# Optimization experiments

Hardware: AMD Instinct MI355X
Metric: run time of the kernel (lower is better)

## Reference

```python
import jax, jax.numpy as jnp
import numpy as np
import math

T = 4096
HID = 2048
H = 16
D = 128
RD = 64            # rotary_dim = head_dim * partial_rotary_factor (0.5)
THETA = 10000.0
EPS = 1e-6
GROUPS = 8
LAYER_IDX = 2
N_LAYERS = 32


def build_slope_tensor(num_heads):
    def get_slopes_power_of_2(n):
        start = 2 ** (-(2 ** (-(math.log2(n) - 3))))
        ratio = start
        return [start * ratio ** i for i in range(n)]
    if math.log2(num_heads).is_integer():
        return get_slopes_power_of_2(num_heads)
    closest = 2 ** math.floor(math.log2(num_heads))
    return (get_slopes_power_of_2(closest)
            + build_slope_tensor(2 * closest)[0::2][: num_heads - closest])


def compute_slope():
    base = np.array(build_slope_tensor(H), dtype=np.float32)
    return jnp.asarray(-base * (1 - (LAYER_IDX - 1) / (N_LAYERS - 1) + 1e-5), dtype=jnp.float32)


def setup_inputs() -> dict:
    key = jax.random.key(0)
    ks = jax.random.split(key, 8)
    s = 0.02
    return {
        "positions": jnp.arange(T, dtype=jnp.int32),
        "hidden_states": jax.random.normal(ks[0], (T, HID), dtype=jnp.float32),
        "recurrent_state": jnp.zeros((1, H, D, D), dtype=jnp.float32),
        "w_qkv": jax.random.normal(ks[1], (HID, 3 * H * D), dtype=jnp.float32) * s,
        "w_g": jax.random.normal(ks[2], (HID, H * D), dtype=jnp.float32) * s,
        "w_dense": jax.random.normal(ks[3], (H * D, HID), dtype=jnp.float32) * s,
        "q_norm_w": jnp.ones((D,), dtype=jnp.float32),
        "k_norm_w": jnp.ones((D,), dtype=jnp.float32),
        "g_norm_w": jnp.ones((H * D,), dtype=jnp.float32),
    }


def _rms(x, w):
    var = jnp.mean(jnp.square(x), axis=-1, keepdims=True)
    return x * jax.lax.rsqrt(var + EPS) * w


def _rope(x, positions):
    # partial neox-style rotary on first RD dims of each head
    inv_freq = 1.0 / (THETA ** (jnp.arange(0, RD, 2, dtype=jnp.float32) / RD))
    freqs = positions.astype(jnp.float32)[:, None] * inv_freq   # [T, RD/2]
    cos = jnp.cos(freqs)[:, None, :]                            # [T, 1, RD/2]
    sin = jnp.sin(freqs)[:, None, :]
    x1 = x[..., : RD // 2]
    x2 = x[..., RD // 2 : RD]
    x_pass = x[..., RD:]
    return jnp.concatenate([x1 * cos - x2 * sin, x2 * cos + x1 * sin, x_pass], axis=-1)


def reference(positions, hidden_states, recurrent_state,
              w_qkv, w_g, w_dense, q_norm_w, k_norm_w, g_norm_w):
    t = hidden_states.shape[0]
    qkv = (hidden_states @ w_qkv).reshape(t, 3, H, D)
    q, k, v = qkv[:, 0], qkv[:, 1], qkv[:, 2]
    q = _rms(q, q_norm_w)
    k = _rms(k, k_norm_w)
    q = _rope(q, positions)
    k = _rope(k, positions)

    slope = compute_slope()                    # [H], negative
    decay = jnp.exp(slope)                     # per-head per-step decay
    scale = D ** -0.5
    q = (q * scale).astype(jnp.float32)
    k = k.astype(jnp.float32)
    v = v.astype(jnp.float32)

    def step(S, qkv_t):
        q_t, k_t, v_t = qkv_t                  # each [H, D]
        S = S * decay[:, None, None] + k_t[:, :, None] * v_t[:, None, :]
        o_t = jnp.einsum('hk,hkv->hv', q_t, S)
        return S, o_t

    S0 = recurrent_state[0].astype(jnp.float32)   # [H, K, V]
    S_final, o = jax.lax.scan(step, S0, (q, k, v))
    attn = o.reshape(t, H * D)

    gate = jax.nn.sigmoid(hidden_states @ w_g)
    # GroupRMSNorm: normalize per group of size (H*D)/GROUPS, scale by full weight
    g = attn.reshape(t, GROUPS, (H * D) // GROUPS)
    var = jnp.mean(jnp.square(g), axis=-1, keepdims=True)
    g = (g * jax.lax.rsqrt(var + EPS)).reshape(t, H * D) * g_norm_w

    out = (g * gate) @ w_dense
    return out, S_final[None]
```

## Files before the change

### kernel.cpp

```cpp
#include <hip/hip_runtime.h>
#include <hip/hip_bf16.h>

using bf16x8 = __attribute__((ext_vector_type(8))) __bf16;
using f32x4  = __attribute__((ext_vector_type(4))) float;

constexpr int T_SEQ = 4096;
constexpr int HID_C = 2048;
constexpr int NH    = 16;
constexpr int QKV_N = 6144;

__device__ __forceinline__ float head_slope(int h) {
    return -exp2f(-0.5f * (float)(h + 1)) * 0.967751935483871f;
}

__device__ __forceinline__ ushort f2bfu(float f) {
    __hip_bfloat16 h = __float2bfloat16(f);
    return *(ushort*)&h;
}
__device__ __forceinline__ float bfu2f(ushort u) {
    union { unsigned int i; float f; } x; x.i = ((unsigned int)u) << 16; return x.f;
}

__device__ __forceinline__ void async16(const ushort* g, ushort* l) {
    __builtin_amdgcn_global_load_lds((const __attribute__((address_space(1))) void*)g,
                                     (__attribute__((address_space(3))) void*)l, 16, 0, 0);
}

template<int N> __device__ __forceinline__ void waitcnt_vm() {
    if constexpr (N == 0)      asm volatile("s_waitcnt vmcnt(0)" ::: "memory");
    else if constexpr (N == 2) asm volatile("s_waitcnt vmcnt(2)" ::: "memory");
    else if constexpr (N == 4) asm volatile("s_waitcnt vmcnt(4)" ::: "memory");
    else if constexpr (N == 6) asm volatile("s_waitcnt vmcnt(6)" ::: "memory");
}

__device__ __forceinline__ void cvt_body(const float* __restrict__ src, ushort* __restrict__ dst,
                                         int bid, int tid) {
    int i = (bid * 256 + tid) * 8;
    float4 a = *(const float4*)(src + i);
    float4 b = *(const float4*)(src + i + 4);
    ushort4 ua = {f2bfu(a.x), f2bfu(a.y), f2bfu(a.z), f2bfu(a.w)};
    ushort4 ub = {f2bfu(b.x), f2bfu(b.y), f2bfu(b.z), f2bfu(b.w)};
    *(ushort4*)(dst + i) = ua;
    *(ushort4*)(dst + i + 4) = ub;
}

__device__ __forceinline__ void transpose_body(const float* __restrict__ src,
                                               ushort* __restrict__ dst,
                                               int R, int C, int bx, int by, int t,
                                               ushort (*tile)[68]) {
    int tr = by * 64, tc = bx * 64;
    int r0 = t >> 4;
    int c4 = (t & 15) << 2;
#pragma unroll
    for (int p = 0; p < 4; ++p) {
        int row = r0 + p * 16;
        float4 v = *(const float4*)&src[(size_t)(tr + row) * C + tc + c4];
        tile[row][c4 + 0] = f2bfu(v.x);
        tile[row][c4 + 1] = f2bfu(v.y);
        tile[row][c4 + 2] = f2bfu(v.z);
        tile[row][c4 + 3] = f2bfu(v.w);
    }
    __syncthreads();
#pragma unroll
    for (int p = 0; p < 4; ++p) {
        int orow = r0 + p * 16;
        ushort4 u;
        u.x = tile[c4 + 0][orow];
        u.y = tile[c4 + 1][orow];
        u.z = tile[c4 + 2][orow];
        u.w = tile[c4 + 3][orow];
        *(ushort4*)&dst[(size_t)(tc + orow) * R + tr + c4] = u;
    }
}

__global__ __launch_bounds__(256) void prep_all(const float* __restrict__ hidden,
                                                ushort* __restrict__ hid_b,
                                                const float* __restrict__ w_qkv,
                                                ushort* __restrict__ wqkv_t,
                                                const float* __restrict__ w_g,
                                                ushort* __restrict__ wg_t,
                                                const float* __restrict__ w_dense,
                                                ushort* __restrict__ wd_t,
                                                const int* __restrict__ positions,
                                                float2* __restrict__ ropet) {
    __shared__ ushort tile[64][68];
    int b = blockIdx.x, t = threadIdx.x;
    if (b < 4096) {
        cvt_body(hidden, hid_b, b, t);
    } else if (b < 7168) {
        int bb = b - 4096;
        transpose_body(w_qkv, wqkv_t, HID_C, QKV_N, bb % 96, bb / 96, t, tile);
    } else if (b < 8192) {
        int bb = b - 7168;
        transpose_body(w_g, wg_t, HID_C, HID_C, bb % 32, bb / 32, t, tile);
    } else if (b < 9216) {
        int bb = b - 8192;
        transpose_body(w_dense, wd_t, HID_C, HID_C, bb % 32, bb / 32, t, tile);
    } else {
        int i = (b - 9216) * 256 + t;
        int tt = i >> 5, fi = i & 31;
        float inv = expf((float)fi * -0.2878231366f);
        float freq = (float)positions[tt] * inv;
        float sn, cs;
        sincosf(freq, &sn, &cs);
        ropet[i] = make_float2(cs, sn);
    }
}

template<int MI, int BN>
__device__ __forceinline__ void gemm8_core(const ushort* __restrict__ Ag,
                                           const ushort* __restrict__ Bg,
                                           int K, int bm, int bn,
                                           ushort* sh, f32x4 (&acc)[MI][4]) {
    constexpr int WM = 16 / MI;
    constexpr int WN = 8 / WM;
    constexpr int SB = BN / 128;
    constexpr int AH = (MI >= 8) ? 2 : 1;
    constexpr int MH = MI / AH;

    const int tid  = threadIdx.x;
    const int lane = tid & 63;
    const int wave = tid >> 6;
    const int lane15 = lane & 15, quad = lane >> 4;
    const int wm = wave / WN, wn = wave % WN;
    const int swz = lane15 & 7;

    ushort* const ldsA0 = sh;
    ushort* const ldsA1 = sh + 16384;
    ushort* const ldsB0 = sh + 32768;
    ushort* const ldsB1 = sh + 32768 + BN * 64;

    const int srow = lane >> 3;
    const int scol = ((lane & 7) ^ srow) << 3;
    const ushort* gA = Ag + (size_t)(bm + srow) * K + scol;
    const ushort* gB = Bg + (size_t)(bn + srow) * K + scol;
    const int ro  = wave * 16;
    const int roB = wave * 8 * SB;
    const int NT = K >> 6;

#define STAGE_A(L, k0) do { \
    _Pragma("unroll") for (int h = 0; h < 2; ++h) \
    _Pragma("unroll") for (int q = 0; q < 2; ++q) \
        async16(gA + (size_t)((h) * 128 + ro + q * 8) * K + (k0), (L) + ((h) * 128 + ro + q * 8) * 64); } while (0)
#define STAGE_B(L, k0) do { \
    _Pragma("unroll") for (int h = 0; h < 2; ++h) \
    _Pragma("unroll") for (int q = 0; q < SB; ++q) \
        async16(gB + (size_t)((h) * (BN / 2) + roB + q * 8) * K + (k0), (L) + ((h) * (BN / 2) + roB + q * 8) * 64); } while (0)

    STAGE_A(ldsA0, 0);
    STAGE_B(ldsB0, 0);
    waitcnt_vm<0>();
    asm volatile("s_barrier" ::: "memory");

    for (int t = 0; t < NT; ++t) {
        const ushort* LA = (t & 1) ? ldsA1 : ldsA0;
        const ushort* LB = (t & 1) ? ldsB1 : ldsB0;
        ushort* LAn = (t & 1) ? ldsA0 : ldsA1;
        ushort* LBn = (t & 1) ? ldsB0 : ldsB1;
        bf16x8 bfr[4][2];
#pragma unroll
        for (int j = 0; j < 4; ++j)
#pragma unroll
            for (int ks = 0; ks < 2; ++ks)
                bfr[j][ks] = *(const bf16x8*)&LB[(wn * 64 + j * 16 + lane15) * 64 + (((ks * 4 + quad) ^ swz) << 3)];
        bf16x8 af0[MH][2];
#pragma unroll
        for (int i = 0; i < MH; ++i)
#pragma unroll
            for (int ks = 0; ks < 2; ++ks)
                af0[i][ks] = *(const bf16x8*)&LA[(wm * (MI * 16) + i * 16 + lane15) * 64 + (((ks * 4 + quad) ^ swz) << 3)];
        if (t + 1 < NT) {
            STAGE_A(LAn, (t + 1) << 6);
            STAGE_B(LBn, (t + 1) << 6);
        }
        __builtin_amdgcn_s_setprio(1);
#pragma unroll
        for (int i = 0; i < MH; ++i)
#pragma unroll
            for (int j = 0; j < 4; ++j)
#pragma unroll
                for (int ks = 0; ks < 2; ++ks)
                    acc[i][j] = __builtin_amdgcn_mfma_f32_16x16x32_bf16(af0[i][ks], bfr[j][ks], acc[i][j], 0, 0, 0);
        __builtin_amdgcn_s_setprio(0);
        if constexpr (AH == 2) {
            bf16x8 af1[MH][2];
#pragma unroll
            for (int i = 0; i < MH; ++i)
#pragma unroll
                for (int ks = 0; ks < 2; ++ks)
                    af1[i][ks] = *(const bf16x8*)&LA[(wm * (MI * 16) + (MH + i) * 16 + lane15) * 64 + (((ks * 4 + quad) ^ swz) << 3)];
            __builtin_amdgcn_s_setprio(1);
#pragma unroll
            for (int i = 0; i < MH; ++i)
#pragma unroll
                for (int j = 0; j < 4; ++j)
#pragma unroll
                    for (int ks = 0; ks < 2; ++ks)
                        acc[MH + i][j] = __builtin_amdgcn_mfma_f32_16x16x32_bf16(af1[i][ks], bfr[j][ks], acc[MH + i][j], 0, 0, 0);
            __builtin_amdgcn_s_setprio(0);
        }
        waitcnt_vm<0>();
        asm volatile("s_barrier" ::: "memory");
    }
#undef STAGE_A
#undef STAGE_B
}

__device__ __forceinline__ void gemm4_core(const ushort* __restrict__ Ag,
                                           const ushort* __restrict__ Bg,
                                           int K, int bm, int bn,
                                           ushort* sh, f32x4 (&acc)[4][4]) {
    const int tid  = threadIdx.x;
    const int lane = tid & 63;
    const int wave = tid >> 6;
    const int lane15 = lane & 15, quad = lane >> 4;
    const int wm = wave >> 1, wn = wave & 1;
    const int swz = lane15 & 7;

    ushort* const ldsA0 = sh;
    ushort* const ldsA1 = sh + 8192;
    ushort* const ldsB0 = sh + 16384;
    ushort* const ldsB1 = sh + 24576;

    const int srow = lane >> 3;
    const int scol = ((lane & 7) ^ srow) << 3;
    const ushort* gA = Ag + (size_t)(bm + srow) * K + scol;
    const ushort* gB = Bg + (size_t)(bn + srow) * K + scol;
    const int ro = wave * 32;
    const int NT = K >> 6;

#define STG(L, g, k0) do { \
    _Pragma("unroll") for (int q = 0; q < 4; ++q) \
        async16((g) + (size_t)(ro + q * 8) * K + (k0), (L) + (ro + q * 8) * 64); } while (0)

    STG(ldsA0, gA, 0);
    STG(ldsB0, gB, 0);
    waitcnt_vm<0>();
    asm volatile("s_barrier" ::: "memory");

    for (int t = 0; t < NT; ++t) {
        const ushort* LA = (t & 1) ? ldsA1 : ldsA0;
        const ushort* LB = (t & 1) ? ldsB1 : ldsB0;
        ushort* LAn = (t & 1) ? ldsA0 : ldsA1;
        ushort* LBn = (t & 1) ? ldsB0 : ldsB1;
        bf16x8 bfr[4][2];
#pragma unroll
        for (int j = 0; j < 4; ++j)
#pragma unroll
            for (int ks = 0; ks < 2; ++ks)
                bfr[j][ks] = *(const bf16x8*)&LB[(wn * 64 + j * 16 + lane15) * 64 + (((ks * 4 + quad) ^ swz) << 3)];
        bf16x8 af[4][2];
#pragma unroll
        for (int i = 0; i < 4; ++i)
#pragma unroll
            for (int ks = 0; ks < 2; ++ks)
                af[i][ks] = *(const bf16x8*)&LA[(wm * 64 + i * 16 + lane15) * 64 + (((ks * 4 + quad) ^ swz) << 3)];
        if (t + 1 < NT) {
            STG(LAn, gA, (t + 1) << 6);
            STG(LBn, gB, (t + 1) << 6);
        }
        __builtin_amdgcn_s_setprio(1);
#pragma unroll
        for (int i = 0; i < 4; ++i)
#pragma unroll
            for (int j = 0; j < 4; ++j)
#pragma unroll
                for (int ks = 0; ks < 2; ++ks)
                    acc[i][j] = __builtin_amdgcn_mfma_f32_16x16x32_bf16(af[i][ks], bfr[j][ks], acc[i][j], 0, 0, 0);
        __builtin_amdgcn_s_setprio(0);
        waitcnt_vm<0>();
        asm volatile("s_barrier" ::: "memory");
    }
#undef STG
}

__global__ __launch_bounds__(512, 2) void gemm_fused(const ushort* __restrict__ A,
                                                     const ushort* __restrict__ Bcat,
                                                     ushort* __restrict__ qkv,
                                                     ushort* __restrict__ gate,
                                                     ushort* __restrict__ vT, int K) {
    __shared__ ushort sh[65536];
    int bid = blockIdx.x;
    int x = bid & 7, w = bid >> 3;
    int rm = x >> 2, rn = x & 3;
    int wm_i = w >> 3, wn_i = w & 7;
    int bm = (rm * 8 + wm_i) * 256;
    int bn = (rn * 8 + wn_i) * 256;
    f32x4 acc[8][4] = {};
    gemm8_core<8, 256>(A, Bcat, K, bm, bn, sh, acc);

    int lane = threadIdx.x & 63, wave = threadIdx.x >> 6;
    int lane15 = lane & 15, quad = lane >> 4;
    int wm = wave >> 2, wn = wave & 3;

    if (bn >= 4096 && bn < QKV_N) {
        constexpr int S = 132;
        ushort* L = sh;
        int h0 = (bn - 4096) >> 7;
        int c0 = bm >> 7;
        int hq = wn >> 1;
        int dl = (wn & 1) * 64;
#pragma unroll
        for (int cq = 0; cq < 2; ++cq) {
            if (wm == cq) {
#pragma unroll
                for (int i = 0; i < 8; ++i)
#pragma unroll
                    for (int j = 0; j < 4; ++j) {
                        int d_local = dl + j * 16 + lane15;
#pragma unroll
                        for (int r = 0; r < 4; ++r) {
                            int t_local = i * 16 + quad * 4 + r;
                            L[hq * 128 * S + d_local * S + t_local] = f2bfu(acc[i][j][r]);
                        }
                    }
            }
            __syncthreads();
#pragma unroll
            for (int p = 0; p < 16; ++p) {
                int lin = (p * 512 + threadIdx.x) * 4;
                int hq2 = lin >> 14;
                int wi = lin & 16383;
                int d = wi >> 7, t4 = wi & 127;
                const ushort* lp = &L[hq2 * 128 * S + d * S + t4];
                ushort4 u = { lp[0], lp[1], lp[2], lp[3] };
                *(ushort4*)&vT[((size_t)((h0 + hq2) * 32 + c0 + cq) * 128 + d) * 128 + t4] = u;
            }
            __syncthreads();
        }
        return;
    }

    bool isg = bn >= QKV_N;
    ushort* outp = isg ? gate : qkv;
    int ncol = isg ? HID_C : QKV_N;
    int cb = (isg ? bn - QKV_N : bn) + wn * 64;
    int rb = bm + wm * 128;
#pragma unroll
    for (int i = 0; i < 8; ++i)
#pragma unroll
        for (int j = 0; j < 4; ++j) {
            int col = cb + j * 16 + lane15;
#pragma unroll
            for (int r = 0; r < 4; ++r) {
                float v = acc[i][j][r];
                if (isg) v = 1.0f / (1.0f + __expf(-v));
                outp[(size_t)(rb + i * 16 + quad * 4 + r) * ncol + col] = f2bfu(v);
            }
        }
}

__global__ __launch_bounds__(256, 2) void gemm_dense(const ushort* __restrict__ A,
                                                     const ushort* __restrict__ Bt,
                                                     float* __restrict__ Cout, int N, int K) {
    __shared__ ushort sh[32768];
    int bid = blockIdx.x;
    int x = bid & 7, w = bid >> 3;
    int rm = x >> 1, rn = x & 1;
    int wm_i = w >> 3, wn_i = w & 7;
    int bm = (rm * 8 + wm_i) * 128;
    int bn = (rn * 8 + wn_i) * 128;
    f32x4 acc[4][4] = {};
    gemm4_core(A, Bt, K, bm, bn, sh, acc);

    int lane = threadIdx.x & 63, wave = threadIdx.x >> 6;
    int lane15 = lane & 15, quad = lane >> 4;
    int wm = wave >> 1, wn = wave & 1;
    int cb = bn + wn * 64;
    int rb = bm + wm * 64;
#pragma unroll
    for (int i = 0; i < 4; ++i)
#pragma unroll
        for (int j = 0; j < 4; ++j) {
            int col = cb + j * 16 + lane15;
#pragma unroll
            for (int r = 0; r < 4; ++r)
                Cout[(size_t)(rb + i * 16 + quad * 4 + r) * N + col] = acc[i][j][r];
        }
}

__global__ __launch_bounds__(256) void qk_rope_T(ushort* __restrict__ qkv,
                                                 const float2* __restrict__ tab,
                                                 const float* __restrict__ qw,
                                                 const float* __restrict__ kw,
                                                 ushort* __restrict__ kT) {
    __shared__ ushort tile[64][132];
    int bt = blockIdx.x;
    int kind = blockIdx.y >> 4, h = blockIdx.y & 15;
    int tid = threadIdx.x;
    int row = tid >> 2, c = tid & 3, d0 = c * 32;
    int t = bt * 64 + row;
    ushort* base = qkv + (size_t)t * QKV_N + kind * 2048 + h * 128 + d0;
    bf16x8 pk[4];
#pragma unroll
    for (int p = 0; p < 4; ++p) pk[p] = *(const bf16x8*)(base + p * 8);
    {
        float x[32];
        float ss = 0.f;
#pragma unroll
        for (int p = 0; p < 4; ++p)
#pragma unroll
            for (int i = 0; i < 8; ++i) {
                x[p * 8 + i] = (float)pk[p][i];
                ss += x[p * 8 + i] * x[p * 8 + i];
            }
        ss += __shfl_xor(ss, 1);
        ss += __shfl_xor(ss, 2);
        float rr = rsqrtf(ss * (1.0f / 128.0f) + 1e-6f);
        const float* w = (kind == 0) ? qw : kw;
#pragma unroll
        for (int i = 0; i < 32; ++i) x[i] *= rr * w[d0 + i];
#pragma unroll
        for (int i = 0; i < 32; ++i) {
            float p = __shfl_xor(x[i], 1);
            if (c < 2) {
                float2 rt = tab[t * 32 + i];
                x[i] = (c == 0) ? (x[i] * rt.x - p * rt.y) : (x[i] * rt.x + p * rt.y);
            }
        }
        float sc = (kind == 0) ? 0.08838834764831845f : 1.0f;
#pragma unroll
        for (int p = 0; p < 4; ++p)
#pragma unroll
            for (int i = 0; i < 8; ++i) pk[p][i] = (__bf16)(x[p * 8 + i] * sc);
#pragma unroll
        for (int p = 0; p < 4; ++p) *(bf16x8*)(base + p * 8) = pk[p];
    }
    if (kind == 1) {
#pragma unroll
        for (int p = 0; p < 4; ++p) {
            ushort4* s = (ushort4*)&pk[p];
            *(ushort4*)&tile[row][d0 + p * 8]     = s[0];
            *(ushort4*)&tile[row][d0 + p * 8 + 4] = s[1];
        }
        __syncthreads();
        ushort* outT = kT + ((size_t)(h * 32 + (bt >> 1)) * 128) * 128 + (bt & 1) * 64;
        int d = tid >> 1, half = tid & 1;
#pragma unroll
        for (int tt = 0; tt < 8; ++tt) {
            int tl = half * 32 + tt * 4;
            ushort4 u;
            u.x = tile[tl + 0][d];
            u.y = tile[tl + 1][d];
            u.z = tile[tl + 2][d];
            u.w = tile[tl + 3][d];
            *(ushort4*)&outT[(size_t)d * 128 + tl] = u;
        }
    }
}

__global__ __launch_bounds__(256) void chunk_partial(const ushort* __restrict__ kT,
                                                     const ushort* __restrict__ vT,
                                                     ushort* __restrict__ PT) {
    int c = blockIdx.x, h = blockIdx.y;
    float slope = head_slope(h);
    float lam_inv = __expf(-slope);
    int tid = threadIdx.x, lane = tid & 63, wave = tid >> 6;
    int lane15 = lane & 15, quad = lane >> 4;
    int wv = (wave & 1) * 64, wd = (wave >> 1) * 64;
    const ushort* vbase = vT + ((size_t)(h * 32 + c) * 128) * 128;
    const ushort* kbase = kT + ((size_t)(h * 32 + c) * 128) * 128;
    f32x4 acc[4][4] = {};
#pragma unroll
    for (int j0 = 0; j0 < 128; j0 += 32) {
        float w8[8];
        w8[0] = __expf(slope * (float)(127 - (j0 + quad * 8)));
#pragma unroll
        for (int kk = 1; kk < 8; ++kk) w8[kk] = w8[kk - 1] * lam_inv;
        bf16x8 afr[4], bfr[4];
#pragma unroll
        for (int i = 0; i < 4; ++i) {
            bf16x8 v = *(const bf16x8*)&vbase[(size_t)(wv + i * 16 + lane15) * 128 + j0 + quad * 8];
#pragma unroll
            for (int kk = 0; kk < 8; ++kk) afr[i][kk] = (__bf16)((float)v[kk] * w8[kk]);
        }
#pragma unroll
        for (int j = 0; j < 4; ++j)
            bfr[j] = *(const bf16x8*)&kbase[(size_t)(wd + j * 16 + lane15) * 128 + j0 + quad * 8];
#pragma unroll
        for (int i = 0; i < 4; ++i)
#pragma unroll
            for (int j = 0; j < 4; ++j)
                acc[i][j] = __builtin_amdgcn_mfma_f32_16x16x32_bf16(afr[i], bfr[j], acc[i][j], 0, 0, 0);
    }
    ushort* out = PT + ((size_t)c * 16 + h) * 16384;
#pragma unroll
    for (int i = 0; i < 4; ++i)
#pragma unroll
        for (int j = 0; j < 4; ++j)
#pragma unroll
            for (int r = 0; r < 4; ++r)
                out[(size_t)(wv + i * 16 + quad * 4 + r) * 128 + wd + j * 16 + lane15] = f2bfu(acc[i][j][r]);
}

__global__ __launch_bounds__(128) void scan_states(const ushort* __restrict__ PT,
                                                   const float* __restrict__ S0,
                                                   ushort* __restrict__ Spb,
                                                   float* __restrict__ Sfin) {
    int hv = blockIdx.x;
    int d = threadIdx.x;
    int h = hv >> 7, v = hv & 127;
    float lamC = __expf(head_slope(h) * 128.0f);
    float s = S0[(size_t)h * 16384 + d * 128 + v];
#pragma unroll
    for (int c = 0; c < 32; ++c) {
        size_t idx = ((size_t)c * 2048 + hv) * 128 + d;
        Spb[idx] = f2bfu(s);
        s = s * lamC + bfu2f(PT[idx]);
    }
    Sfin[(size_t)h * 16384 + d * 128 + v] = s;
}

__global__ __launch_bounds__(256) void chunk_out(const ushort* __restrict__ qkv,
                                                 const ushort* __restrict__ vT,
                                                 const ushort* __restrict__ Spb,
                                                 ushort* __restrict__ o) {
    int c = blockIdx.x, h = blockIdx.y;
    float slope = head_slope(h);
    __shared__ ushort Ps[128 * 136];
    int tid = threadIdx.x, lane = tid & 63, wave = tid >> 6;
    int lane15 = lane & 15, quad = lane >> 4;
    int t0 = c * 128;
    int tt0 = wave, tt1 = 7 - wave;
    const ushort* qbase = qkv + (size_t)t0 * QKV_N + h * 128;
    const ushort* kbase = qbase + 2048;

    bf16x8 qf0[4], qf1[4];
#pragma unroll
    for (int ds = 0; ds < 4; ++ds) {
        qf0[ds] = *(const bf16x8*)&qbase[(size_t)(tt0 * 16 + lane15) * QKV_N + ds * 32 + quad * 8];
        qf1[ds] = *(const bf16x8*)&qbase[(size_t)(tt1 * 16 + lane15) * QKV_N + ds * 32 + quad * 8];
    }
    f32x4 s0a[4] = {};
    f32x4 s1a[8] = {};
#pragma unroll
    for (int st = 0; st < 8; ++st) {
        if (st <= tt1) {
            bf16x8 kf[4];
#pragma unroll
            for (int ds = 0; ds < 4; ++ds)
                kf[ds] = *(const bf16x8*)&kbase[(size_t)(st * 16 + lane15) * QKV_N + ds * 32 + quad * 8];
#pragma unroll
            for (int ds = 0; ds < 4; ++ds)
                s1a[st] = __builtin_amdgcn_mfma_f32_16x16x32_bf16(qf1[ds], kf[ds], s1a[st], 0, 0, 0);
            if (st <= tt0) {
#pragma unroll
                for (int ds = 0; ds < 4; ++ds)
                    s0a[st] = __builtin_amdgcn_mfma_f32_16x16x32_bf16(qf0[ds], kf[ds], s0a[st], 0, 0, 0);
            }
        }
    }
    int stmax0 = tt0 + ((tt0 & 1) ? 0 : 1);
    int stmax1 = tt1 + ((tt1 & 1) ? 0 : 1);
#pragma unroll
    for (int st = 0; st < 8; ++st) {
        if (st <= stmax1) {
#pragma unroll
            for (int r = 0; r < 4; ++r) {
                int t = tt1 * 16 + quad * 4 + r;
                int s = st * 16 + lane15;
                float val = 0.f;
                if (st <= tt1) val = (s <= t) ? s1a[st][r] * __expf(slope * (float)(t - s)) : 0.f;
                Ps[t * 136 + s] = f2bfu(val);
            }
        }
    }
#pragma unroll
    for (int st = 0; st < 5; ++st) {
        if (st <= stmax0) {
#pragma unroll
            for (int r = 0; r < 4; ++r) {
                int t = tt0 * 16 + quad * 4 + r;
                int s = st * 16 + lane15;
                float val = 0.f;
                if (st <= tt0) val = (s <= t) ? s0a[st][r] * __expf(slope * (float)(t - s)) : 0.f;
                Ps[t * 136 + s] = f2bfu(val);
            }
        }
    }
    __syncthreads();
    f32x4 oa0[8] = {};
    f32x4 oa1[8] = {};
    float lam0 = __expf(slope * (float)(tt0 * 16 + lane15 + 1));
    float lam1 = __expf(slope * (float)(tt1 * 16 + lane15 + 1));
    bf16x8 qs0[4], qs1[4];
#pragma unroll
    for (int ds = 0; ds < 4; ++ds)
#pragma unroll
        for (int kk = 0; kk < 8; ++kk) {
            qs0[ds][kk] = (__bf16)((float)qf0[ds][kk] * lam0);
            qs1[ds][kk] = (__bf16)((float)qf1[ds][kk] * lam1);
        }
    const ushort* spb = Spb + ((size_t)c * 2048 + h * 128) * 128;
#pragma unroll
    for (int vt = 0; vt < 8; ++vt)
#pragma unroll
        for (int ds = 0; ds < 4; ++ds) {
            bf16x8 bfrag = *(const bf16x8*)&spb[(vt * 16 + lane15) * 128 + ds * 32 + quad * 8];
            oa0[vt] = __builtin_amdgcn_mfma_f32_16x16x32_bf16(qs0[ds], bfrag, oa0[vt], 0, 0, 0);
            oa1[vt] = __builtin_amdgcn_mfma_f32_16x16x32_bf16(qs1[ds], bfrag, oa1[vt], 0, 0, 0);
        }
    const ushort* vbase = vT + ((size_t)(h * 32 + c) * 128) * 128;
    int ns0 = (tt0 + 2) >> 1, ns1 = (tt1 + 2) >> 1;
#pragma unroll
    for (int s32 = 0; s32 < 4; ++s32) {
        if (s32 < ns1) {
            bf16x8 af = *(const bf16x8*)&Ps[(tt1 * 16 + lane15) * 136 + s32 * 32 + quad * 8];
#pragma unroll
            for (int vt = 0; vt < 8; ++vt) {
                bf16x8 bfrag = *(const bf16x8*)&vbase[(size_t)(vt * 16 + lane15) * 128 + s32 * 32 + quad * 8];
                oa1[vt] = __builtin_amdgcn_mfma_f32_16x16x32_bf16(af, bfrag, oa1[vt], 0, 0, 0);
            }
        }
    }
#pragma unroll
    for (int s32 = 0; s32 < 2; ++s32) {
        if (s32 < ns0) {
            bf16x8 af = *(const bf16x8*)&Ps[(tt0 * 16 + lane15) * 136 + s32 * 32 + quad * 8];
#pragma unroll
            for (int vt = 0; vt < 8; ++vt) {
                bf16x8 bfrag = *(const bf16x8*)&vbase[(size_t)(vt * 16 + lane15) * 128 + s32 * 32 + quad * 8];
                oa0[vt] = __builtin_amdgcn_mfma_f32_16x16x32_bf16(af, bfrag, oa0[vt], 0, 0, 0);
            }
        }
    }
#pragma unroll
    for (int vt = 0; vt < 8; ++vt)
#pragma unroll
        for (int r = 0; r < 4; ++r) {
            o[(size_t)(t0 + tt0 * 16 + quad * 4 + r) * 2048 + h * 128 + vt * 16 + lane15] = f2bfu(oa0[vt][r]);
            o[(size_t)(t0 + tt1 * 16 + quad * 4 + r) * 2048 + h * 128 + vt * 16 + lane15] = f2bfu(oa1[vt][r]);
        }
}

__global__ __launch_bounds__(256) void gnorm_gate(const ushort* __restrict__ o,
                                                  const ushort* __restrict__ gate,
                                                  const float* __restrict__ gw,
                                                  ushort* __restrict__ gg) {
    int t = blockIdx.x;
    int tid = threadIdx.x;
    const ushort* op = o + (size_t)t * 2048 + tid * 8;
    bf16x8 xv = *(const bf16x8*)op;
    float x[8];
    float ss = 0.0f;
#pragma unroll
    for (int i = 0; i < 8; ++i) { x[i] = (float)xv[i]; ss += x[i] * x[i]; }
#pragma unroll
    for (int off = 16; off > 0; off >>= 1) ss += __shfl_xor(ss, off);
    float r = rsqrtf(ss * (1.0f / 256.0f) + 1e-6f);
    const ushort* gp = gate + (size_t)t * 2048;
#pragma unroll
    for (int i = 0; i < 8; ++i) {
        int j = tid * 8 + i;
        float val = x[i] * r * gw[j] * bfu2f(gp[j]);
        gg[(size_t)t * 2048 + j] = f2bfu(val);
    }
}

extern "C" void kernel_launch(void* const* d_in, const int* in_sizes, int n_in,
                              void* d_out, int out_size, void* d_ws, size_t ws_size,
                              hipStream_t stream) {
    const int* positions   = (const int*)d_in[0];
    const float* hidden    = (const float*)d_in[1];
    const float* S0        = (const float*)d_in[2];
    const float* w_qkv     = (const float*)d_in[3];
    const float* w_g       = (const float*)d_in[4];
    const float* w_dense   = (const float*)d_in[5];
    const float* qw        = (const float*)d_in[6];
    const float* kw        = (const float*)d_in[7];
    const float* gw        = (const float*)d_in[8];

    char* ws = (char*)d_ws;
    ushort* qkv     = (ushort*)ws;
    ushort* wqkv_t  = (ushort*)(ws + 50331648);
    ushort* wg_t    = (ushort*)(ws + 75497472);
    float2* ropet   = (float2*)(ws + 159383552);
    ushort* PT      = (ushort*)(ws + 50331648);
    ushort* wd_t    = (ushort*)(ws + 83886080);
    ushort* gatebuf = (ushort*)(ws + 92274688);
    ushort* hid_b   = (ushort*)(ws + 109051904);
    ushort* Spb     = (ushort*)(ws + 109051904);
    ushort* kT      = (ushort*)(ws + 125829120);
    ushort* vT      = (ushort*)(ws + 142606336);
    ushort* gg      = (ushort*)ws;

    float* out  = (float*)d_out;
    float* Sfin = out + (size_t)T_SEQ * HID_C;
    ushort* obuf = (ushort*)d_out;

    prep_all<<<9728, 256, 0, stream>>>(hidden, hid_b, w_qkv, wqkv_t, w_g, wg_t,
                                       w_dense, wd_t, positions, ropet);

    gemm_fused<<<dim3(512), 512, 0, stream>>>(hid_b, wqkv_t, qkv, gatebuf, vT, HID_C);

    qk_rope_T<<<dim3(T_SEQ / 64, 32), 256, 0, stream>>>(qkv, ropet, qw, kw, kT);

    chunk_partial<<<dim3(32, 16), 256, 0, stream>>>(kT, vT, PT);
    scan_states<<<2048, 128, 0, stream>>>(PT, S0, Spb, Sfin);
    chunk_out<<<dim3(32, 16), 256, 0, stream>>>(qkv, vT, Spb, obuf);
    gnorm_gate<<<T_SEQ, 256, 0, stream>>>(obuf, gatebuf, gw, gg);

    gemm_dense<<<dim3(512), 256, 0, stream>>>(gg, wd_t, out, HID_C, HID_C);
}
```

Before: 420.0 us.

## Fuse QK RMSNorm, RoPE and K transpose into QKV GEMM epilogue

Moves per-head RMS normalization, partial rotary embedding, q scaling and the K transpose into the epilogue of the fused QKV/gate GEMM, and removes the separate qk_rope_T kernel. The head-wide sum of squares is reduced with lane shuffles and exchanged between paired waves through shared memory. This drops one launch and a full read-modify-write pass over q and k. In exchange the GEMM epilogue gets longer, adds barriers, and may raise register pressure.

```diff
diff --git a/kernel.cpp b/kernel.cpp
--- a/kernel.cpp
+++ b/kernel.cpp
@@ -278,7 +278,11 @@
                                                      const ushort* __restrict__ Bcat,
                                                      ushort* __restrict__ qkv,
                                                      ushort* __restrict__ gate,
-                                                     ushort* __restrict__ vT, int K) {
+                                                     ushort* __restrict__ kT,
+                                                     ushort* __restrict__ vT,
+                                                     const float2* __restrict__ tab,
+                                                     const float* __restrict__ qw,
+                                                     const float* __restrict__ kw, int K) {
     __shared__ ushort sh[65536];
     int bid = blockIdx.x;
     int x = bid & 7, w = bid >> 3;
@@ -292,9 +296,100 @@
     int lane = threadIdx.x & 63, wave = threadIdx.x >> 6;
     int lane15 = lane & 15, quad = lane >> 4;
     int wm = wave >> 2, wn = wave & 3;
-
-    if (bn >= 4096 && bn < QKV_N) {
-        constexpr int S = 132;
+    constexpr int S = 132;
+
+    if (bn < 4096) {
+        bool isq = bn < 2048;
+        const float* wnorm = isq ? qw : kw;
+        int hq = wn >> 1, dl = (wn & 1) * 64;
+        int rowbase = bm + wm * 128;
+        float w4[4];
+#pragma unroll
+        for (int j = 0; j < 4; ++j) w4[j] = wnorm[dl + j * 16 + lane15];
+        float* ssb = (float*)&sh[63488];
+#pragma unroll
+        for (int i = 0; i < 8; ++i)
+#pragma unroll
+            for (int r = 0; r < 4; ++r) {
+                float s2 = 0.f;
+#pragma unroll
+                for (int j = 0; j < 4; ++j) { float xv = acc[i][j][r]; s2 += xv * xv; }
+                s2 += __shfl_xor(s2, 1);
+                s2 += __shfl_xor(s2, 2);
+                s2 += __shfl_xor(s2, 4);
+                s2 += __shfl_xor(s2, 8);
+                if (lane15 == 0) ssb[wave * 128 + i * 16 + quad * 4 + r] = s2;
+            }
+        __syncthreads();
+        float sc = isq ? 0.08838834764831845f : 1.0f;
+#pragma unroll
+        for (int i = 0; i < 8; ++i)
+#pragma unroll
+            for (int r = 0; r < 4; ++r) {
+                int row = i * 16 + quad * 4 + r;
+                float ssf = ssb[wave * 128 + row] + ssb[(wave ^ 1) * 128 + row];
+                float rr = rsqrtf(ssf * (1.0f / 128.0f) + 1e-6f);
+                float xx[4];
+#pragma unroll
+                for (int j = 0; j < 4; ++j) xx[j] = acc[i][j][r] * rr * w4[j];
+                if (dl == 0) {
+                    int t = rowbase + row;
+                    float2 rt0 = tab[t * 32 + lane15];
+                    float2 rt1 = tab[t * 32 + 16 + lane15];
+                    float a0 = xx[0], b0 = xx[2], a1 = xx[1], b1 = xx[3];
+                    xx[0] = a0 * rt0.x - b0 * rt0.y;
+                    xx[2] = b0 * rt0.x + a0 * rt0.y;
+                    xx[1] = a1 * rt1.x - b1 * rt1.y;
+                    xx[3] = b1 * rt1.x + a1 * rt1.y;
+                }
+#pragma unroll
+                for (int j = 0; j < 4; ++j) acc[i][j][r] = xx[j] * sc;
+            }
+#pragma unroll
+        for (int i = 0; i < 8; ++i)
+#pragma unroll
+            for (int j = 0; j < 4; ++j) {
+                int col = bn + wn * 64 + j * 16 + lane15;
+#pragma unroll
+                for (int r = 0; r < 4; ++r)
+                    qkv[(size_t)(rowbase + i * 16 + quad * 4 + r) * QKV_N + col] = f2bfu(acc[i][j][r]);
+            }
+        if (!isq) {
+            ushort* L = sh;
+            int h0 = (bn - 2048) >> 7;
+            int c0 = bm >> 7;
+            __syncthreads();
+#pragma unroll
+            for (int cq = 0; cq < 2; ++cq) {
+                if (wm == cq) {
+#pragma unroll
+                    for (int i = 0; i < 8; ++i)
+#pragma unroll
+                        for (int j = 0; j < 4; ++j) {
+                            int d_local = dl + j * 16 + lane15;
+#pragma unroll
+                            for (int r = 0; r < 4; ++r)
+                                L[hq * 128 * S + d_local * S + i * 16 + quad * 4 + r] = f2bfu(acc[i][j][r]);
+                        }
+                }
+                __syncthreads();
+#pragma unroll
+                for (int p = 0; p < 16; ++p) {
+                    int lin = (p * 512 + threadIdx.x) * 4;
+                    int hq2 = lin >> 14;
+                    int wi = lin & 16383;
+                    int d = wi >> 7, t4 = wi & 127;
+                    const ushort* lp = &L[hq2 * 128 * S + d * S + t4];
+                    ushort4 u = { lp[0], lp[1], lp[2], lp[3] };
+                    *(ushort4*)&kT[((size_t)((h0 + hq2) * 32 + c0 + cq) * 128 + d) * 128 + t4] = u;
+                }
+                __syncthreads();
+            }
+        }
+        return;
+    }
+
+    if (bn < QKV_N) {
         ushort* L = sh;
         int h0 = (bn - 4096) >> 7;
         int c0 = bm >> 7;
@@ -309,10 +404,8 @@
                     for (int j = 0; j < 4; ++j) {
                         int d_local = dl + j * 16 + lane15;
 #pragma unroll
-                        for (int r = 0; r < 4; ++r) {
-                            int t_local = i * 16 + quad * 4 + r;
-                            L[hq * 128 * S + d_local * S + t_local] = f2bfu(acc[i][j][r]);
-                        }
+                        for (int r = 0; r < 4; ++r)
+                            L[hq * 128 * S + d_local * S + i * 16 + quad * 4 + r] = f2bfu(acc[i][j][r]);
                     }
             }
             __syncthreads();
@@ -331,10 +424,7 @@
         return;
     }
 
-    bool isg = bn >= QKV_N;
-    ushort* outp = isg ? gate : qkv;
-    int ncol = isg ? HID_C : QKV_N;
-    int cb = (isg ? bn - QKV_N : bn) + wn * 64;
+    int cb = (bn - QKV_N) + wn * 64;
     int rb = bm + wm * 128;
 #pragma unroll
     for (int i = 0; i < 8; ++i)
@@ -343,9 +433,8 @@
             int col = cb + j * 16 + lane15;
 #pragma unroll
             for (int r = 0; r < 4; ++r) {
-                float v = acc[i][j][r];
-                if (isg) v = 1.0f / (1.0f + __expf(-v));
-                outp[(size_t)(rb + i * 16 + quad * 4 + r) * ncol + col] = f2bfu(v);
+                float v = 1.0f / (1.0f + __expf(-acc[i][j][r]));
+                gate[(size_t)(rb + i * 16 + quad * 4 + r) * HID_C + col] = f2bfu(v);
             }
         }
 }
@@ -377,76 +466,6 @@
             for (int r = 0; r < 4; ++r)
                 Cout[(size_t)(rb + i * 16 + quad * 4 + r) * N + col] = acc[i][j][r];
         }
-}
-
-__global__ __launch_bounds__(256) void qk_rope_T(ushort* __restrict__ qkv,
-                                                 const float2* __restrict__ tab,
-                                                 const float* __restrict__ qw,
-                                                 const float* __restrict__ kw,
-                                                 ushort* __restrict__ kT) {
-    __shared__ ushort tile[64][132];
-    int bt = blockIdx.x;
-    int kind = blockIdx.y >> 4, h = blockIdx.y & 15;
-    int tid = threadIdx.x;
-    int row = tid >> 2, c = tid & 3, d0 = c * 32;
-    int t = bt * 64 + row;
-    ushort* base = qkv + (size_t)t * QKV_N + kind * 2048 + h * 128 + d0;
-    bf16x8 pk[4];
-#pragma unroll
-    for (int p = 0; p < 4; ++p) pk[p] = *(const bf16x8*)(base + p * 8);
-    {
-        float x[32];
-        float ss = 0.f;
-#pragma unroll
-        for (int p = 0; p < 4; ++p)
-#pragma unroll
-            for (int i = 0; i < 8; ++i) {
-                x[p * 8 + i] = (float)pk[p][i];
-                ss += x[p * 8 + i] * x[p * 8 + i];
-            }
-        ss += __shfl_xor(ss, 1);
-        ss += __shfl_xor(ss, 2);
-        float rr = rsqrtf(ss * (1.0f / 128.0f) + 1e-6f);
-        const float* w = (kind == 0) ? qw : kw;
-#pragma unroll
-        for (int i = 0; i < 32; ++i) x[i] *= rr * w[d0 + i];
-#pragma unroll
-        for (int i = 0; i < 32; ++i) {
-            float p = __shfl_xor(x[i], 1);
-            if (c < 2) {
-                float2 rt = tab[t * 32 + i];
-                x[i] = (c == 0) ? (x[i] * rt.x - p * rt.y) : (x[i] * rt.x + p * rt.y);
-            }
-        }
-        float sc = (kind == 0) ? 0.08838834764831845f : 1.0f;
-#pragma unroll
-        for (int p = 0; p < 4; ++p)
-#pragma unroll
-            for (int i = 0; i < 8; ++i) pk[p][i] = (__bf16)(x[p * 8 + i] * sc);
-#pragma unroll
-        for (int p = 0; p < 4; ++p) *(bf16x8*)(base + p * 8) = pk[p];
-    }
-    if (kind == 1) {
-#pragma unroll
-        for (int p = 0; p < 4; ++p) {
-            ushort4* s = (ushort4*)&pk[p];
-            *(ushort4*)&tile[row][d0 + p * 8]     = s[0];
-            *(ushort4*)&tile[row][d0 + p * 8 + 4] = s[1];
-        }
-        __syncthreads();
-        ushort* outT = kT + ((size_t)(h * 32 + (bt >> 1)) * 128) * 128 + (bt & 1) * 64;
-        int d = tid >> 1, half = tid & 1;
-#pragma unroll
-        for (int tt = 0; tt < 8; ++tt) {
-            int tl = half * 32 + tt * 4;
-            ushort4 u;
-            u.x = tile[tl + 0][d];
-            u.y = tile[tl + 1][d];
-            u.z = tile[tl + 2][d];
-            u.w = tile[tl + 3][d];
-            *(ushort4*)&outT[(size_t)d * 128 + tl] = u;
-        }
-    }
 }
 
 __global__ __launch_bounds__(256) void chunk_partial(const ushort* __restrict__ kT,
@@ -691,9 +710,8 @@
     prep_all<<<9728, 256, 0, stream>>>(hidden, hid_b, w_qkv, wqkv_t, w_g, wg_t,
                                        w_dense, wd_t, positions, ropet);
 
-    gemm_fused<<<dim3(512), 512, 0, stream>>>(hid_b, wqkv_t, qkv, gatebuf, vT, HID_C);
-
-    qk_rope_T<<<dim3(T_SEQ / 64, 32), 256, 0, stream>>>(qkv, ropet, qw, kw, kT);
+    gemm_fused<<<dim3(512), 512, 0, stream>>>(hid_b, wqkv_t, qkv, gatebuf, kT, vT,
+                                              ropet, qw, kw, HID_C);
 
     chunk_partial<<<dim3(32, 16), 256, 0, stream>>>(kT, vT, PT);
     scan_states<<<2048, 128, 0, stream>>>(PT, S0, Spb, Sfin);
```

Result: faster. 409.6 us (-2.5%).
